# Performance work log

Hardware: AMD Instinct MI355X
Metric: run time of the kernel (lower is better)

The kernel has to match this reference:

```python
import jax, jax.numpy as jnp
import numpy as np

D = 512      # slot_dim
DP = 128     # pairwise_dim
H = 8        # num_heads
HD = D // H  # head_dim
EPS = 1e-5


def layernorm(x, w, b):
    mu = jnp.mean(x, axis=-1, keepdims=True)
    var = jnp.var(x, axis=-1, keepdims=True)
    return (x - mu) * jax.lax.rsqrt(var + EPS) * w + b


def setup_inputs() -> dict:
    key = jax.random.key(0)
    ks = jax.random.split(key, 12)
    B, K = 4, 512
    s = 0.02
    return {
        "slots": jax.random.normal(ks[0], (B, K, D), jnp.float32),
        "pairwise": jax.random.normal(ks[1], (B, K, K, DP), jnp.float32),
        "ln1_w": jnp.ones((D,), jnp.float32),
        "ln1_b": jnp.zeros((D,), jnp.float32),
        "ln2_w": jnp.ones((D,), jnp.float32),
        "ln2_b": jnp.zeros((D,), jnp.float32),
        "w_qkv": jax.random.normal(ks[2], (D, 3 * D), jnp.float32) * s,
        "edge_w": jax.random.normal(ks[3], (DP, H), jnp.float32) * s,
        "edge_b": jnp.zeros((H,), jnp.float32),
        "out_w": jax.random.normal(ks[4], (D, D), jnp.float32) * s,
        "out_b": jnp.zeros((D,), jnp.float32),
        "ffn_w1": jax.random.normal(ks[5], (D, 4 * D), jnp.float32) * s,
        "ffn_b1": jnp.zeros((4 * D,), jnp.float32),
        "ffn_w2": jax.random.normal(ks[6], (4 * D, D), jnp.float32) * s,
        "ffn_b2": jnp.zeros((D,), jnp.float32),
    }


def reference(slots, pairwise, ln1_w, ln1_b, ln2_w, ln2_b, w_qkv,
              edge_w, edge_b, out_w, out_b, ffn_w1, ffn_b1, ffn_w2, ffn_b2):
    B, K, _ = slots.shape
    x = layernorm(slots, ln1_w, ln1_b)
    qkv = x @ w_qkv                                   # (B,K,3D)
    q, k, v = jnp.split(qkv, 3, axis=-1)
    # (B,K,D) -> (B,H,K,HD)
    split = lambda t: t.reshape(B, K, H, HD).transpose(0, 2, 1, 3)
    q, k, v = split(q), split(k), split(v)
    attn = jnp.einsum('bhqd,bhkd->bhqk', q, k) * (HD ** -0.5)
    edge_bias = jnp.einsum('bqkp,ph->bhqk', pairwise, edge_w) + edge_b[None, :, None, None]
    attn = jax.nn.softmax(attn + edge_bias, axis=-1)
    out = jnp.einsum('bhqk,bhkd->bhqd', attn, v)      # (B,H,K,HD)
    out = out.transpose(0, 2, 1, 3).reshape(B, K, D)
    slots = slots + out @ out_w + out_b
    y = layernorm(slots, ln2_w, ln2_b)
    h = jax.nn.gelu(y @ ffn_w1 + ffn_b1, approximate=False)
    slots = slots + h @ ffn_w2 + ffn_b2
    return slots
```

## Files before the change

### kernel.cpp

```cpp
#include <hip/hip_runtime.h>
#include <hip/hip_bf16.h>

typedef __attribute__((ext_vector_type(8))) short bf16x8;
typedef __attribute__((ext_vector_type(4))) float f32x4;

#define DEV __device__ __forceinline__

DEV float ldf(const float* p){ return *p; }
DEV float ldf(const unsigned short* p){ return __uint_as_float(((unsigned)*p) << 16); }
DEV void stout(float* p, float v){ *p = v; }
DEV void stout(unsigned short* p, float v){
  __hip_bfloat16 h = __float2bfloat16(v);
  *p = *reinterpret_cast<unsigned short*>(&h);
}
DEV unsigned short bf16bits(float v){
  __hip_bfloat16 h = __float2bfloat16(v);
  return *reinterpret_cast<unsigned short*>(&h);
}

__global__ __launch_bounds__(256) void ln_kernel(const float* __restrict__ in,
    const float* __restrict__ w, const float* __restrict__ bb,
    unsigned short* __restrict__ out)
{
  const int row = blockIdx.x;
  const int tid = threadIdx.x;
  const long base = (long)row * 512;
  float v0 = in[base + tid];
  float v1 = in[base + 256 + tid];
  float s = v0 + v1, ss = v0*v0 + v1*v1;
  #pragma unroll
  for (int o = 32; o > 0; o >>= 1){ s += __shfl_down(s, o); ss += __shfl_down(ss, o); }
  __shared__ float rA[4], rB[4];
  const int wid = tid >> 6, lid = tid & 63;
  if (lid == 0){ rA[wid] = s; rB[wid] = ss; }
  __syncthreads();
  s  = rA[0] + rA[1] + rA[2] + rA[3];
  ss = rB[0] + rB[1] + rB[2] + rB[3];
  float mu  = s * (1.f/512.f);
  float var = ss * (1.f/512.f) - mu*mu;
  float r   = rsqrtf(var + 1e-5f);
  stout(&out[base + tid],       (v0 - mu) * r * w[tid]       + bb[tid]);
  stout(&out[base + 256 + tid], (v1 - mu) * r * w[256 + tid] + bb[256 + tid]);
}

template<typename TIN>
__global__ __launch_bounds__(256) void transpose_conv(
    const TIN* __restrict__ in, unsigned short* __restrict__ out,
    int ldin, int ldout, long sIn, long sOut)
{
  __shared__ float t[32][33];
  in  += (long)blockIdx.z * sIn;
  out += (long)blockIdx.z * sOut;
  const int n0 = blockIdx.x*32, k0 = blockIdx.y*32;
  const int c = threadIdx.x & 31, r0 = threadIdx.x >> 5;
  #pragma unroll
  for (int i = 0; i < 4; i++){
    int r = r0 + i*8;
    t[r][c] = ldf(&in[(long)(k0 + r)*ldin + n0 + c]);
  }
  __syncthreads();
  #pragma unroll
  for (int i = 0; i < 4; i++){
    int r = r0 + i*8;
    stout(&out[(long)(n0 + r)*ldout + k0 + c], t[c][r]);
  }
}

template<int MT,int NT,int WGM,int WGN,int WR,int WC,int EPI,typename TOUT,int BDIV>
__global__ __launch_bounds__(256) void mfma_gemm(
    const unsigned short* __restrict__ A, const unsigned short* __restrict__ B,
    TOUT* __restrict__ C,
    int lda, int ldb, int ldc, int Kd,
    long sA, long sA2, long sB, long sB2, long sC, long sC2,
    const float* __restrict__ bias, const float* __restrict__ res)
{
  const int bz = blockIdx.z;
  A += (long)(bz / BDIV) * sA + (long)(bz % BDIV) * sA2;
  B += (long)(bz / BDIV) * sB + (long)(bz % BDIV) * sB2;
  C += (long)(bz / BDIV) * sC + (long)(bz % BDIV) * sC2;
  if (res) res += (long)(bz / BDIV) * sC + (long)(bz % BDIV) * sC2;
  __shared__ unsigned short As[MT][40];
  __shared__ unsigned short Bs[NT][40];
  const int tid  = threadIdx.x;
  const int lane = tid & 63, wv = tid >> 6;
  const int quad = lane >> 4, l16 = lane & 15;
  const int wm = (wv % WGM) * WR * 16;
  const int wn = (wv / WGM) * WC * 16;
  const int m0 = blockIdx.y * MT, n0 = blockIdx.x * NT;
  f32x4 acc[WR][WC] = {};
  for (int k0 = 0; k0 < Kd; k0 += 32){
    #pragma unroll
    for (int it = 0; it < MT*32/(256*8); ++it){
      int idx = (it*256 + tid) * 8;
      int r = idx >> 5, c = idx & 31;
      *(uint4*)&As[r][c] = *(const uint4*)&A[(long)(m0 + r)*lda + k0 + c];
    }
    #pragma unroll
    for (int it = 0; it < NT*32/(256*8); ++it){
      int idx = (it*256 + tid) * 8;
      int r = idx >> 5, c = idx & 31;
      *(uint4*)&Bs[r][c] = *(const uint4*)&B[(long)(n0 + r)*ldb + k0 + c];
    }
    __syncthreads();
    bf16x8 af[WR], bfr[WC];
    #pragma unroll
    for (int i = 0; i < WR; i++) af[i]  = *(const bf16x8*)&As[wm + i*16 + l16][quad*8];
    #pragma unroll
    for (int j = 0; j < WC; j++) bfr[j] = *(const bf16x8*)&Bs[wn + j*16 + l16][quad*8];
    #pragma unroll
    for (int i = 0; i < WR; i++)
      #pragma unroll
      for (int j = 0; j < WC; j++)
        acc[i][j] = __builtin_amdgcn_mfma_f32_16x16x32_bf16(af[i], bfr[j], acc[i][j], 0, 0, 0);
    __syncthreads();
  }
  #pragma unroll
  for (int i = 0; i < WR; i++){
    #pragma unroll
    for (int j = 0; j < WC; j++){
      #pragma unroll
      for (int r = 0; r < 4; r++){
        int m = m0 + wm + i*16 + quad*4 + r;
        int n = n0 + wn + j*16 + l16;
        float v = acc[i][j][r];
        long idx = (long)m * ldc + n;
        if (EPI == 0){ stout(&C[idx], v); }
        else if (EPI == 2){ stout(&C[idx], v + bias[n] + res[idx]); }
        else if (EPI == 3){
          v += bias[n];
          v = 0.5f * v * (1.f + erff(v * 0.70710678118f));
          stout(&C[idx], v);
        }
      }
    }
  }
}

__global__ __launch_bounds__(256) void edge_bias_kernel(
    const float* __restrict__ pw,
    const float* __restrict__ edge_w,
    const float* __restrict__ edge_b,
    float* __restrict__ scores)
{
  const int tid  = threadIdx.x;
  const int lane = tid & 63;
  const int wid  = tid >> 6;
  const int sub  = lane & 15;
  const int quad = lane >> 4;
  float ew[8][8];
  #pragma unroll
  for (int j = 0; j < 8; j++)
    #pragma unroll
    for (int h = 0; h < 8; h++)
      ew[j][h] = edge_w[(sub*8 + j)*8 + h];
  const int b3 = (sub >> 3) & 1, b2_ = (sub >> 2) & 1, b1 = (sub >> 1) & 1;
  const int myh = b3*4 + b2_*2 + b1;
  const float ebh = edge_b[myh];
  const long total = 1048576;
  for (long base = (long)blockIdx.x * 16; base < total; base += (long)gridDim.x * 16){
    long pair = base + wid*4 + quad;
    const float* src = pw + pair * 128 + sub * 8;
    float4 r0 = *reinterpret_cast<const float4*>(src);
    float4 r1 = *reinterpret_cast<const float4*>(src + 4);
    float x[8] = {r0.x, r0.y, r0.z, r0.w, r1.x, r1.y, r1.z, r1.w};
    float acc[8] = {0,0,0,0,0,0,0,0};
    #pragma unroll
    for (int j = 0; j < 8; j++)
      #pragma unroll
      for (int h = 0; h < 8; h++)
        acc[h] += x[j] * ew[j][h];
    float t[4];
    #pragma unroll
    for (int i = 0; i < 4; i++){
      float send = b3 ? acc[i] : acc[i+4];
      float keep = b3 ? acc[i+4] : acc[i];
      t[i] = keep + __shfl_xor(send, 8);
    }
    float u[2];
    #pragma unroll
    for (int i = 0; i < 2; i++){
      float send = b2_ ? t[i] : t[i+2];
      float keep = b2_ ? t[i+2] : t[i];
      u[i] = keep + __shfl_xor(send, 4);
    }
    float send = b1 ? u[0] : u[1];
    float keep = b1 ? u[1] : u[0];
    float val = keep + __shfl_xor(send, 2);
    val += __shfl_xor(val, 1);
    if ((sub & 1) == 0){
      long b  = pair >> 18;
      long qk = pair & 262143;
      scores[(b*8 + myh) * 262144 + qk] = val + ebh;
    }
  }
}

__global__ __launch_bounds__(256) void fused_attn(
    const unsigned short* __restrict__ qkv,
    const float* __restrict__ bias,
    const unsigned short* __restrict__ vt,
    unsigned short* __restrict__ attn_out)
{
  __shared__ unsigned short Qs[64][72];
  __shared__ unsigned short Ks[128][72];
  __shared__ unsigned short Vs[64][136];
  __shared__ unsigned short Ps[64][136];
  const int q0 = blockIdx.x * 64;
  const int h  = blockIdx.y;
  const int b  = blockIdx.z;
  const int tid  = threadIdx.x;
  const int lane = tid & 63, w = tid >> 6;
  const int l16  = lane & 15, quad = lane >> 4;

  const unsigned short* Qg = qkv + (long)(b*512 + q0)*1536 + h*64;
  const unsigned short* Kg = qkv + (long)(b*512)*1536 + 512 + h*64;
  const unsigned short* Vg = vt  + (long)b*262144 + (long)(h*64)*512;
  const float*          Bg = bias + ((long)(b*8 + h)*512 + q0)*512;

  #pragma unroll
  for (int it = 0; it < 2; ++it){
    int idx = (it*256 + tid)*8; int r = idx >> 6, c = idx & 63;
    *(uint4*)&Qs[r][c] = *(const uint4*)&Qg[(long)r*1536 + c];
  }
  __syncthreads();
  bf16x8 aq[2];
  aq[0] = *(const bf16x8*)&Qs[w*16 + l16][quad*8];
  aq[1] = *(const bf16x8*)&Qs[w*16 + l16][32 + quad*8];

  float m_run[4] = {-1e30f, -1e30f, -1e30f, -1e30f};
  float l_run[4] = {0.f, 0.f, 0.f, 0.f};
  f32x4 on[4] = {};

  for (int kt = 0; kt < 4; ++kt){
    const int k0 = kt * 128;
    __syncthreads();
    #pragma unroll
    for (int it = 0; it < 4; ++it){
      int idx = (it*256 + tid)*8; int r = idx >> 6, c = idx & 63;
      *(uint4*)&Ks[r][c] = *(const uint4*)&Kg[(long)(k0 + r)*1536 + c];
    }
    #pragma unroll
    for (int it = 0; it < 4; ++it){
      int idx = (it*256 + tid)*8; int r = idx >> 7, c = idx & 127;
      *(uint4*)&Vs[r][c] = *(const uint4*)&Vg[(long)r*512 + k0 + c];
    }
    float bb[4][8];
    #pragma unroll
    for (int r = 0; r < 4; ++r){
      const float* bp = Bg + (long)(w*16 + quad*4 + r)*512 + k0 + l16;
      #pragma unroll
      for (int j = 0; j < 8; ++j) bb[r][j] = bp[16*j];
    }
    __syncthreads();
    f32x4 sacc[8] = {};
    #pragma unroll
    for (int j = 0; j < 8; ++j){
      bf16x8 bk0 = *(const bf16x8*)&Ks[j*16 + l16][quad*8];
      bf16x8 bk1 = *(const bf16x8*)&Ks[j*16 + l16][32 + quad*8];
      sacc[j] = __builtin_amdgcn_mfma_f32_16x16x32_bf16(aq[0], bk0, sacc[j], 0, 0, 0);
      sacc[j] = __builtin_amdgcn_mfma_f32_16x16x32_bf16(aq[1], bk1, sacc[j], 0, 0, 0);
    }
    #pragma unroll
    for (int r = 0; r < 4; ++r){
      float s[8];
      #pragma unroll
      for (int j = 0; j < 8; ++j) s[j] = fmaf(sacc[j][r], 0.125f, bb[r][j]);
      float tm = s[0];
      #pragma unroll
      for (int j = 1; j < 8; ++j) tm = fmaxf(tm, s[j]);
      #pragma unroll
      for (int o = 1; o < 16; o <<= 1) tm = fmaxf(tm, __shfl_xor(tm, o));
      float mnew  = fmaxf(m_run[r], tm);
      float alpha = __expf(m_run[r] - mnew);
      m_run[r] = mnew;
      float ps = 0.f;
      #pragma unroll
      for (int j = 0; j < 8; ++j){
        float p = __expf(s[j] - mnew);
        ps += p;
        Ps[w*16 + quad*4 + r][l16 + 16*j] = bf16bits(p);
      }
      #pragma unroll
      for (int o = 1; o < 16; o <<= 1) ps += __shfl_xor(ps, o);
      l_run[r] = l_run[r] * alpha + ps;
      #pragma unroll
      for (int n = 0; n < 4; ++n) on[n][r] *= alpha;
    }
    #pragma unroll
    for (int ks = 0; ks < 4; ++ks){
      bf16x8 pa = *(const bf16x8*)&Ps[w*16 + l16][ks*32 + quad*8];
      #pragma unroll
      for (int n = 0; n < 4; ++n){
        bf16x8 bv = *(const bf16x8*)&Vs[n*16 + l16][ks*32 + quad*8];
        on[n] = __builtin_amdgcn_mfma_f32_16x16x32_bf16(pa, bv, on[n], 0, 0, 0);
      }
    }
  }
  unsigned short* Og = attn_out + (long)(b*512 + q0)*512 + h*64;
  #pragma unroll
  for (int r = 0; r < 4; ++r){
    float inv = 1.f / l_run[r];
    #pragma unroll
    for (int n = 0; n < 4; ++n)
      Og[(long)(w*16 + quad*4 + r)*512 + n*16 + l16] = bf16bits(on[n][r] * inv);
  }
}

extern "C" void kernel_launch(void* const* d_in, const int* in_sizes, int n_in,
                              void* d_out, int out_size, void* d_ws, size_t ws_size,
                              hipStream_t stream)
{
  const float* slots    = (const float*)d_in[0];
  const float* pairwise = (const float*)d_in[1];
  const float* ln1_w    = (const float*)d_in[2];
  const float* ln1_b    = (const float*)d_in[3];
  const float* ln2_w    = (const float*)d_in[4];
  const float* ln2_b    = (const float*)d_in[5];
  const float* w_qkv    = (const float*)d_in[6];
  const float* edge_w   = (const float*)d_in[7];
  const float* edge_b   = (const float*)d_in[8];
  const float* out_w    = (const float*)d_in[9];
  const float* out_b    = (const float*)d_in[10];
  const float* ffn_w1   = (const float*)d_in[11];
  const float* ffn_b1   = (const float*)d_in[12];
  const float* ffn_w2   = (const float*)d_in[13];
  const float* ffn_b2   = (const float*)d_in[14];
  float* out = (float*)d_out;

  float* ws      = (float*)d_ws;
  float* scores  = ws;
  float* slots2  = ws + 8388608;
  unsigned short* ub = (unsigned short*)(ws + 9437184);
  unsigned short* x_b    = ub;
  unsigned short* qkv_b  = ub + 1048576;
  unsigned short* vt_b   = ub + 12582912;
  unsigned short* attn_b = ub + 13631488;
  unsigned short* y_b    = ub + 14680064;
  unsigned short* h_b    = ub + 15728640;
  unsigned short* wqkvT  = ub + 19922944;
  unsigned short* outwT  = ub + 20709376;
  unsigned short* w1T    = ub + 20971520;
  unsigned short* w2T    = ub + 22020096;

  transpose_conv<float><<<dim3(48,16,1), 256, 0, stream>>>(w_qkv,  wqkvT, 1536, 512, 0, 0);
  transpose_conv<float><<<dim3(16,16,1), 256, 0, stream>>>(out_w,  outwT, 512,  512, 0, 0);
  transpose_conv<float><<<dim3(64,16,1), 256, 0, stream>>>(ffn_w1, w1T,   2048, 512, 0, 0);
  transpose_conv<float><<<dim3(16,64,1), 256, 0, stream>>>(ffn_w2, w2T,   512, 2048, 0, 0);

  ln_kernel<<<2048, 256, 0, stream>>>(slots, ln1_w, ln1_b, x_b);
  mfma_gemm<128,128,2,2,4,4,0,unsigned short,1><<<dim3(12,16,1), 256, 0, stream>>>(
      x_b, wqkvT, qkv_b, 512, 512, 1536, 512,
      0,0,0,0,0,0, nullptr, nullptr);
  edge_bias_kernel<<<8192, 256, 0, stream>>>(pairwise, edge_w, edge_b, scores);
  transpose_conv<unsigned short><<<dim3(16,16,4), 256, 0, stream>>>(
      qkv_b + 1024, vt_b, 1536, 512, 786432, 262144);
  fused_attn<<<dim3(8,8,4), 256, 0, stream>>>(qkv_b, scores, vt_b, attn_b);
  mfma_gemm<64,128,1,4,4,2,2,float,1><<<dim3(4,32,1), 256, 0, stream>>>(
      attn_b, outwT, slots2, 512, 512, 512, 512,
      0,0,0,0,0,0, out_b, slots);
  ln_kernel<<<2048, 256, 0, stream>>>(slots2, ln2_w, ln2_b, y_b);
  mfma_gemm<128,128,2,2,4,4,3,unsigned short,1><<<dim3(16,16,1), 256, 0, stream>>>(
      y_b, w1T, h_b, 512, 512, 2048, 512,
      0,0,0,0,0,0, ffn_b1, nullptr);
  mfma_gemm<64,128,1,4,4,2,2,float,1><<<dim3(4,32,1), 256, 0, stream>>>(
      h_b, w2T, out, 2048, 2048, 512, 2048,
      0,0,0,0,0,0, ffn_b2, slots2);
}
```

Before: 862.4 us.

## Store edge-bias scores as fp16, fuse V transpose into QKV GEMM, merge weight transposes

The edge-bias scores tensor (B*H*K*K) is now written and read as fp16 instead of fp32. This halves the traffic of that intermediate between the edge-bias kernel and the attention kernel. The QKV GEMM epilogue also writes the transposed V directly, which removes a separate transpose launch. The four weight-transpose launches are merged into one kernel. The risks are fp16 rounding error in the bias and uncoalesced strided stores in the V-transpose epilogue.

Measured after the change: 856.9 us, median of 2. Within noise of the previous version (-0.6%).

```diff
diff --git a/kernel.cpp b/kernel.cpp
--- a/kernel.cpp
+++ b/kernel.cpp
@@ -1,5 +1,6 @@
 #include <hip/hip_runtime.h>
 #include <hip/hip_bf16.h>
+#include <hip/hip_fp16.h>
 
 typedef __attribute__((ext_vector_type(8))) short bf16x8;
 typedef __attribute__((ext_vector_type(4))) float f32x4;
@@ -16,6 +17,14 @@
 DEV unsigned short bf16bits(float v){
   __hip_bfloat16 h = __float2bfloat16(v);
   return *reinterpret_cast<unsigned short*>(&h);
+}
+DEV unsigned short f16bits(float v){
+  __half h = __float2half(v);
+  return *reinterpret_cast<unsigned short*>(&h);
+}
+DEV float f16val(unsigned short u){
+  __half h = *reinterpret_cast<__half*>(&u);
+  return __half2float(h);
 }
 
 __global__ __launch_bounds__(256) void ln_kernel(const float* __restrict__ in,
@@ -43,36 +52,42 @@
   stout(&out[base + 256 + tid], (v1 - mu) * r * w[256 + tid] + bb[256 + tid]);
 }
 
-template<typename TIN>
-__global__ __launch_bounds__(256) void transpose_conv(
-    const TIN* __restrict__ in, unsigned short* __restrict__ out,
-    int ldin, int ldout, long sIn, long sOut)
-{
+__global__ __launch_bounds__(256) void weight_transpose_all(
+    const float* __restrict__ w_qkv, const float* __restrict__ out_w,
+    const float* __restrict__ ffn_w1, const float* __restrict__ ffn_w2,
+    unsigned short* __restrict__ wqkvT, unsigned short* __restrict__ outwT,
+    unsigned short* __restrict__ w1T, unsigned short* __restrict__ w2T)
+{
+  int id = blockIdx.x;
+  const float* in; unsigned short* out; int ldin, ldout, bx, by;
+  if (id < 768)      { in = w_qkv;  out = wqkvT; ldin = 1536; ldout = 512;  bx = id % 48; by = id / 48; }
+  else if (id < 1024){ id -= 768;  in = out_w;  out = outwT; ldin = 512;  ldout = 512;  bx = id % 16; by = id / 16; }
+  else if (id < 2048){ id -= 1024; in = ffn_w1; out = w1T;   ldin = 2048; ldout = 512;  bx = id % 64; by = id / 64; }
+  else               { id -= 2048; in = ffn_w2; out = w2T;   ldin = 512;  ldout = 2048; bx = id % 16; by = id / 16; }
   __shared__ float t[32][33];
-  in  += (long)blockIdx.z * sIn;
-  out += (long)blockIdx.z * sOut;
-  const int n0 = blockIdx.x*32, k0 = blockIdx.y*32;
+  const int n0 = bx*32, k0 = by*32;
   const int c = threadIdx.x & 31, r0 = threadIdx.x >> 5;
   #pragma unroll
   for (int i = 0; i < 4; i++){
     int r = r0 + i*8;
-    t[r][c] = ldf(&in[(long)(k0 + r)*ldin + n0 + c]);
+    t[r][c] = in[(long)(k0 + r)*ldin + n0 + c];
   }
   __syncthreads();
   #pragma unroll
   for (int i = 0; i < 4; i++){
     int r = r0 + i*8;
-    stout(&out[(long)(n0 + r)*ldout + k0 + c], t[c][r]);
-  }
-}
-
-template<int MT,int NT,int WGM,int WGN,int WR,int WC,int EPI,typename TOUT,int BDIV>
+    out[(long)(n0 + r)*ldout + k0 + c] = bf16bits(t[c][r]);
+  }
+}
+
+template<int MT,int NT,int WGM,int WGN,int WR,int WC,int EPI,typename TOUT,int BDIV,int VT>
 __global__ __launch_bounds__(256) void mfma_gemm(
     const unsigned short* __restrict__ A, const unsigned short* __restrict__ B,
     TOUT* __restrict__ C,
     int lda, int ldb, int ldc, int Kd,
     long sA, long sA2, long sB, long sB2, long sC, long sC2,
-    const float* __restrict__ bias, const float* __restrict__ res)
+    const float* __restrict__ bias, const float* __restrict__ res,
+    unsigned short* __restrict__ vtout)
 {
   const int bz = blockIdx.z;
   A += (long)(bz / BDIV) * sA + (long)(bz % BDIV) * sA2;
@@ -131,6 +146,10 @@
           v = 0.5f * v * (1.f + erff(v * 0.70710678118f));
           stout(&C[idx], v);
         }
+        if (VT && n0 >= 1024){
+          long vidx = (long)(m >> 9) * 262144 + (long)(n - 1024) * 512 + (m & 511);
+          vtout[vidx] = bf16bits(v);
+        }
       }
     }
   }
@@ -140,7 +159,7 @@
     const float* __restrict__ pw,
     const float* __restrict__ edge_w,
     const float* __restrict__ edge_b,
-    float* __restrict__ scores)
+    unsigned short* __restrict__ scores)
 {
   const int tid  = threadIdx.x;
   const int lane = tid & 63;
@@ -190,14 +209,14 @@
     if ((sub & 1) == 0){
       long b  = pair >> 18;
       long qk = pair & 262143;
-      scores[(b*8 + myh) * 262144 + qk] = val + ebh;
+      scores[(b*8 + myh) * 262144 + qk] = f16bits(val + ebh);
     }
   }
 }
 
 __global__ __launch_bounds__(256) void fused_attn(
     const unsigned short* __restrict__ qkv,
-    const float* __restrict__ bias,
+    const unsigned short* __restrict__ bias,
     const unsigned short* __restrict__ vt,
     unsigned short* __restrict__ attn_out)
 {
@@ -215,7 +234,7 @@
   const unsigned short* Qg = qkv + (long)(b*512 + q0)*1536 + h*64;
   const unsigned short* Kg = qkv + (long)(b*512)*1536 + 512 + h*64;
   const unsigned short* Vg = vt  + (long)b*262144 + (long)(h*64)*512;
-  const float*          Bg = bias + ((long)(b*8 + h)*512 + q0)*512;
+  const unsigned short* Bg = bias + ((long)(b*8 + h)*512 + q0)*512;
 
   #pragma unroll
   for (int it = 0; it < 2; ++it){
@@ -247,9 +266,9 @@
     float bb[4][8];
     #pragma unroll
     for (int r = 0; r < 4; ++r){
-      const float* bp = Bg + (long)(w*16 + quad*4 + r)*512 + k0 + l16;
-      #pragma unroll
-      for (int j = 0; j < 8; ++j) bb[r][j] = bp[16*j];
+      const unsigned short* bp = Bg + (long)(w*16 + quad*4 + r)*512 + k0 + l16;
+      #pragma unroll
+      for (int j = 0; j < 8; ++j) bb[r][j] = f16val(bp[16*j]);
     }
     __syncthreads();
     f32x4 sacc[8] = {};
@@ -328,11 +347,11 @@
   float* out = (float*)d_out;
 
   float* ws      = (float*)d_ws;
-  float* scores  = ws;
-  float* slots2  = ws + 8388608;
-  unsigned short* ub = (unsigned short*)(ws + 9437184);
+  float* slots2  = ws;
+  unsigned short* ub = (unsigned short*)(ws + 1048576);
   unsigned short* x_b    = ub;
   unsigned short* qkv_b  = ub + 1048576;
+  unsigned short* scores = ub + 4194304;
   unsigned short* vt_b   = ub + 12582912;
   unsigned short* attn_b = ub + 13631488;
   unsigned short* y_b    = ub + 14680064;
@@ -342,27 +361,22 @@
   unsigned short* w1T    = ub + 20971520;
   unsigned short* w2T    = ub + 22020096;
 
-  transpose_conv<float><<<dim3(48,16,1), 256, 0, stream>>>(w_qkv,  wqkvT, 1536, 512, 0, 0);
-  transpose_conv<float><<<dim3(16,16,1), 256, 0, stream>>>(out_w,  outwT, 512,  512, 0, 0);
-  transpose_conv<float><<<dim3(64,16,1), 256, 0, stream>>>(ffn_w1, w1T,   2048, 512, 0, 0);
-  transpose_conv<float><<<dim3(16,64,1), 256, 0, stream>>>(ffn_w2, w2T,   512, 2048, 0, 0);
-
+  weight_transpose_all<<<3072, 256, 0, stream>>>(
+      w_qkv, out_w, ffn_w1, ffn_w2, wqkvT, outwT, w1T, w2T);
   ln_kernel<<<2048, 256, 0, stream>>>(slots, ln1_w, ln1_b, x_b);
-  mfma_gemm<128,128,2,2,4,4,0,unsigned short,1><<<dim3(12,16,1), 256, 0, stream>>>(
+  mfma_gemm<128,128,2,2,4,4,0,unsigned short,1,1><<<dim3(12,16,1), 256, 0, stream>>>(
       x_b, wqkvT, qkv_b, 512, 512, 1536, 512,
-      0,0,0,0,0,0, nullptr, nullptr);
+      0,0,0,0,0,0, nullptr, nullptr, vt_b);
   edge_bias_kernel<<<8192, 256, 0, stream>>>(pairwise, edge_w, edge_b, scores);
-  transpose_conv<unsigned short><<<dim3(16,16,4), 256, 0, stream>>>(
-      qkv_b + 1024, vt_b, 1536, 512, 786432, 262144);
   fused_attn<<<dim3(8,8,4), 256, 0, stream>>>(qkv_b, scores, vt_b, attn_b);
-  mfma_gemm<64,128,1,4,4,2,2,float,1><<<dim3(4,32,1), 256, 0, stream>>>(
+  mfma_gemm<64,128,1,4,4,2,2,float,1,0><<<dim3(4,32,1), 256, 0, stream>>>(
       attn_b, outwT, slots2, 512, 512, 512, 512,
-      0,0,0,0,0,0, out_b, slots);
+      0,0,0,0,0,0, out_b, slots, nullptr);
   ln_kernel<<<2048, 256, 0, stream>>>(slots2, ln2_w, ln2_b, y_b);
-  mfma_gemm<128,128,2,2,4,4,3,unsigned short,1><<<dim3(16,16,1), 256, 0, stream>>>(
+  mfma_gemm<128,128,2,2,4,4,3,unsigned short,1,0><<<dim3(16,16,1), 256, 0, stream>>>(
       y_b, w1T, h_b, 512, 512, 2048, 512,
-      0,0,0,0,0,0, ffn_b1, nullptr);
-  mfma_gemm<64,128,1,4,4,2,2,float,1><<<dim3(4,32,1), 256, 0, stream>>>(
+      0,0,0,0,0,0, ffn_b1, nullptr, nullptr);
+  mfma_gemm<64,128,1,4,4,2,2,float,1,0><<<dim3(4,32,1), 256, 0, stream>>>(
       h_b, w2T, out, 2048, 2048, 512, 2048,
-      0,0,0,0,0,0, ffn_b2, slots2);
-}
+      0,0,0,0,0,0, ffn_b2, slots2, nullptr);
+}
```
